# Kernel optimization log

Hardware: AMD Instinct MI355X
Metric: run time of the kernel (lower is better)

## Reference

```python
import jax, jax.numpy as jnp
import numpy as np

DIM = 3072
KV_DIM = 2048
HEADS = 16
DIM_HEAD = 128
INNER = HEADS * DIM_HEAD  # 2048
EPS = 1e-5


def layer_norm(x, g, b):
    mu = jnp.mean(x, axis=-1, keepdims=True)
    var = jnp.var(x, axis=-1, keepdims=True)
    return (x - mu) * jax.lax.rsqrt(var + EPS) * g + b


def setup_inputs() -> dict:
    key = jax.random.key(0)
    ks = jax.random.split(key, 8)
    b, n1, n2 = 2, 2048, 2048
    x = jax.random.normal(ks[0], (b, n1, KV_DIM), dtype=jnp.float32)
    latents = jax.random.normal(ks[1], (b, n2, DIM), dtype=jnp.float32)
    w_q = jax.random.normal(ks[2], (DIM, INNER), dtype=jnp.float32) / np.sqrt(DIM)
    w_kv = jax.random.normal(ks[3], (KV_DIM, 2 * INNER), dtype=jnp.float32) / np.sqrt(KV_DIM)
    w_out = jax.random.normal(ks[4], (INNER, DIM), dtype=jnp.float32) / np.sqrt(INNER)
    ln1_g = jnp.ones((KV_DIM,), jnp.float32)
    ln1_b = jnp.zeros((KV_DIM,), jnp.float32)
    ln2_g = jnp.ones((DIM,), jnp.float32)
    ln2_b = jnp.zeros((DIM,), jnp.float32)
    return {"x": x, "latents": latents, "w_q": w_q, "w_kv": w_kv,
            "w_out": w_out, "ln1_g": ln1_g, "ln1_b": ln1_b,
            "ln2_g": ln2_g, "ln2_b": ln2_b}


def reference(x, latents, w_q, w_kv, w_out, ln1_g, ln1_b, ln2_g, ln2_b):
    b, n2, _ = latents.shape
    xn = layer_norm(x, ln1_g, ln1_b)            # (b, n1, kv_dim)
    ln = layer_norm(latents, ln2_g, ln2_b)      # (b, n2, dim)
    q = ln @ w_q                                # (b, n2, inner)
    kv = xn @ w_kv                              # (b, n1, 2*inner)
    k, v = jnp.split(kv, 2, axis=-1)
    # (b, h, n, d)
    def split_heads(t):
        bs, n, _ = t.shape
        return t.reshape(bs, n, HEADS, DIM_HEAD).transpose(0, 2, 1, 3)
    q, k, v = split_heads(q), split_heads(k), split_heads(v)
    scale = 1.0 / np.sqrt(np.sqrt(DIM_HEAD)).astype(np.float32)
    w = jnp.einsum('bhqd,bhkd->bhqk', q * scale, k * scale)
    w = jax.nn.softmax(w.astype(jnp.float32), axis=-1).astype(q.dtype)
    out = jnp.einsum('bhqk,bhkd->bhqd', w, v)
    out = out.transpose(0, 2, 1, 3).reshape(b, n2, INNER)
    return out @ w_out
```

## Files before the change

kernel.cpp:

```cpp
#include <hip/hip_runtime.h>
#include <type_traits>


using u16 = unsigned short;
using u32 = unsigned int;
typedef __attribute__((ext_vector_type(8))) short short8;
typedef __attribute__((ext_vector_type(4))) float floatx4;

typedef __attribute__((address_space(1))) const unsigned int gu32;
typedef __attribute__((address_space(3))) unsigned int lu32;

__device__ __forceinline__ void gld16(void* lds, const void* g) {
  __builtin_amdgcn_global_load_lds((gu32*)g, (lu32*)lds, 16, 0, 0);
}

__device__ inline u16 f2bf(float f) {
  u32 u = __float_as_uint(f);
  u32 r = (u + 0x7FFFu + ((u >> 16) & 1u)) >> 16;
  return (u16)r;
}

template <int L>
__global__ __launch_bounds__(256) void ln_cast(const float* __restrict__ in,
                                               const float* __restrict__ gw,
                                               const float* __restrict__ bw,
                                               u16* __restrict__ out) {
  constexpr int C4 = L / 1024;
  const int row = blockIdx.x;
  const int t = threadIdx.x;
  const float* rp = in + (size_t)row * L;
  float4 v[C4];
  float s = 0.f, ss = 0.f;
#pragma unroll
  for (int c = 0; c < C4; ++c) {
    v[c] = *(const float4*)(rp + (c * 256 + t) * 4);
    s += v[c].x + v[c].y + v[c].z + v[c].w;
    ss += v[c].x * v[c].x + v[c].y * v[c].y + v[c].z * v[c].z + v[c].w * v[c].w;
  }
#pragma unroll
  for (int off = 32; off > 0; off >>= 1) {
    s += __shfl_down(s, off);
    ss += __shfl_down(ss, off);
  }
  __shared__ float red[8];
  const int wave = t >> 6, lane = t & 63;
  if (lane == 0) { red[wave] = s; red[4 + wave] = ss; }
  __syncthreads();
  const float tot = red[0] + red[1] + red[2] + red[3];
  const float tss = red[4] + red[5] + red[6] + red[7];
  const float mu = tot * (1.f / L);
  const float rstd = rsqrtf(tss * (1.f / L) - mu * mu + 1e-5f);
  u16* op = out + (size_t)row * L;
#pragma unroll
  for (int c = 0; c < C4; ++c) {
    const int base = (c * 256 + t) * 4;
    float4 gv = *(const float4*)(gw + base);
    float4 bv = *(const float4*)(bw + base);
    u32 p0 = (u32)f2bf((v[c].x - mu) * rstd * gv.x + bv.x) |
             ((u32)f2bf((v[c].y - mu) * rstd * gv.y + bv.y) << 16);
    u32 p1 = (u32)f2bf((v[c].z - mu) * rstd * gv.z + bv.z) |
             ((u32)f2bf((v[c].w - mu) * rstd * gv.w + bv.w) << 16);
    uint2 pk; pk.x = p0; pk.y = p1;
    *(uint2*)(op + base) = pk;
  }
}

__global__ __launch_bounds__(256) void transpose_cast(const float* __restrict__ in,
                                                      u16* __restrict__ out,
                                                      int R, int C) {
  __shared__ u16 tile[32][33];
  const int c0 = blockIdx.x * 32, r0 = blockIdx.y * 32;
  const int x = threadIdx.x, y = threadIdx.y;
#pragma unroll
  for (int j = 0; j < 4; ++j)
    tile[y + 8 * j][x] = f2bf(in[(size_t)(r0 + y + 8 * j) * C + c0 + x]);
  __syncthreads();
#pragma unroll
  for (int j = 0; j < 4; ++j)
    out[(size_t)(c0 + y + 8 * j) * R + r0 + x] = tile[x][y + 8 * j];
}

__global__ __launch_bounds__(256) void transpose_v(const u16* __restrict__ kvb,
                                                   u16* __restrict__ vT) {
  __shared__ u16 tile[32][33];
  const int bh = blockIdx.z, b = bh >> 4, h = bh & 15;
  const u16* src = kvb + (size_t)b * 2048 * 4096 + 2048 + h * 128;
  u16* dst = vT + (size_t)bh * 128 * 2048;
  const int d0 = blockIdx.x * 32, n0 = blockIdx.y * 32;
  const int x = threadIdx.x, y = threadIdx.y;
#pragma unroll
  for (int j = 0; j < 4; ++j)
    tile[y + 8 * j][x] = src[(size_t)(n0 + y + 8 * j) * 4096 + d0 + x];
  __syncthreads();
#pragma unroll
  for (int j = 0; j < 4; ++j)
    dst[(size_t)(d0 + y + 8 * j) * 2048 + n0 + x] = tile[x][y + 8 * j];
}

template <typename OutT>
__global__ __launch_bounds__(256) void gemm_bt(const u16* __restrict__ A,
                                               const u16* __restrict__ Bt,
                                               OutT* __restrict__ C,
                                               int M, int N, int K) {
  __shared__ u16 As[128 * 64];
  __shared__ u16 Bs[128 * 64];
  const int tid = threadIdx.x;
  const int wave = tid >> 6, lane = tid & 63, l16 = lane & 15, quad = lane >> 4;
  const int wm = (wave >> 1) * 64, wn = (wave & 1) * 64;
  const long m0 = (long)blockIdx.y * 128, n0 = (long)blockIdx.x * 128;
  const int srow = tid >> 3;
  const int gc = ((tid & 7) ^ ((tid >> 3) & 7)) * 8;
  const u16* Ag0 = A + (m0 + srow) * (long)K + gc;
  const u16* Bg0 = Bt + (n0 + srow) * (long)K + gc;
  const long rowoff = 32L * K;

  const floatx4 fz = {0.f, 0.f, 0.f, 0.f};
  floatx4 acc[4][4];
#pragma unroll
  for (int i = 0; i < 4; ++i)
#pragma unroll
    for (int j = 0; j < 4; ++j) acc[i][j] = fz;

  for (int k0 = 0; k0 < K; k0 += 64) {
    __syncthreads();
#pragma unroll
    for (int c = 0; c < 4; ++c) {
      gld16(&As[(c * 256 + tid) * 8], Ag0 + c * rowoff + k0);
      gld16(&Bs[(c * 256 + tid) * 8], Bg0 + c * rowoff + k0);
    }
    __syncthreads();
#pragma unroll
    for (int kd = 0; kd < 2; ++kd) {
      const int sw = ((4 * kd + quad) ^ (l16 & 7)) * 8;
      short8 a[4], b[4];
#pragma unroll
      for (int i = 0; i < 4; ++i) a[i] = *(const short8*)&As[(wm + i * 16 + l16) * 64 + sw];
#pragma unroll
      for (int j = 0; j < 4; ++j) b[j] = *(const short8*)&Bs[(wn + j * 16 + l16) * 64 + sw];
#pragma unroll
      for (int i = 0; i < 4; ++i)
#pragma unroll
        for (int j = 0; j < 4; ++j)
          acc[i][j] = __builtin_amdgcn_mfma_f32_16x16x32_bf16(a[i], b[j], acc[i][j], 0, 0, 0);
    }
  }

#pragma unroll
  for (int i = 0; i < 4; ++i)
#pragma unroll
    for (int r = 0; r < 4; ++r) {
      const long row = m0 + wm + i * 16 + quad * 4 + r;
#pragma unroll
      for (int j = 0; j < 4; ++j) {
        const long col = n0 + wn + j * 16 + l16;
        if constexpr (std::is_same<OutT, float>::value)
          C[row * N + col] = acc[i][j][r];
        else
          C[row * N + col] = f2bf(acc[i][j][r]);
      }
    }
}

__global__ __launch_bounds__(256, 2) void flash_attn(const u16* __restrict__ Q,
                                                     const u16* __restrict__ KV,
                                                     const u16* __restrict__ VT,
                                                     u16* __restrict__ O) {
  __shared__ u16 Ks[2][64 * 128];
  __shared__ u16 Vs[2][128 * 64];
  __shared__ u16 Ps[4][32 * 64];
  const int tid = threadIdx.x;
  const int wave = tid >> 6, lane = tid & 63, l16 = lane & 15, quad = lane >> 4;
  const int d = blockIdx.x;
  const int bh = (d & 7) * 4 + ((d >> 3) & 3);
  const int qt = d >> 5;
  const int b = bh >> 4, h = bh & 15;
  const u16* Qb = Q + (size_t)b * 2048 * 2048 + h * 128;
  const u16* Kb = KV + (size_t)b * 2048 * 4096 + h * 128;
  const u16* Vb = VT + (size_t)bh * 128 * 2048;
  u16* Ob = O + (size_t)b * 2048 * 2048 + h * 128;
  const int q0 = qt * 128 + wave * 32;

  short8 qf[2][4];
#pragma unroll
  for (int t = 0; t < 2; ++t)
#pragma unroll
    for (int kd = 0; kd < 4; ++kd)
      qf[t][kd] = *(const short8*)&Qb[(size_t)(q0 + t * 16 + l16) * 2048 + kd * 32 + quad * 8];

  short8 onesf;
  {
    union { short8 s; u32 w[4]; } uo;
    const u32 o = (l16 == 0) ? 0x3F803F80u : 0u;
#pragma unroll
    for (int i = 0; i < 4; ++i) uo.w[i] = o;
    onesf = uo.s;
  }

  const floatx4 fz = {0.f, 0.f, 0.f, 0.f};
  floatx4 oacc[2][9];
  float m[2][4];
#pragma unroll
  for (int t = 0; t < 2; ++t) {
#pragma unroll
    for (int jd = 0; jd < 9; ++jd) oacc[t][jd] = fz;
#pragma unroll
    for (int r = 0; r < 4; ++r) m[t][r] = -1e30f;
  }

  u16* Psw = Ps[wave];
  const float sc2 = 0.12751775f;

  auto stage = [&](int buf, int kv0) {
#pragma unroll
    for (int c = 0; c < 4; ++c) {
      const int li = c * 256 + tid;
      const int krow = li >> 4, kdb = (li & 15) ^ (krow & 15);
      gld16(&Ks[buf][li * 8], Kb + (size_t)(kv0 + krow) * 4096 + kdb * 8);
      const int vrow = li >> 3, vdb = (li & 7) ^ (vrow & 7);
      gld16(&Vs[buf][li * 8], Vb + (size_t)vrow * 2048 + kv0 + vdb * 8);
    }
  };

  stage(0, 0);
  int cur = 0;

  for (int kt = 0; kt < 32; ++kt) {
    __syncthreads();
    if (kt < 31) stage(cur ^ 1, (kt + 1) * 64);
    const u16* Kc = Ks[cur];
    const u16* Vc = Vs[cur];

    floatx4 sacc[2][4];
#pragma unroll
    for (int t = 0; t < 2; ++t)
#pragma unroll
      for (int jn = 0; jn < 4; ++jn) sacc[t][jn] = fz;
#pragma unroll
    for (int jn = 0; jn < 4; ++jn)
#pragma unroll
      for (int kd = 0; kd < 4; ++kd) {
        short8 kb = *(const short8*)&Kc[(jn * 16 + l16) * 128 + ((4 * kd + quad) ^ l16) * 8];
        sacc[0][jn] = __builtin_amdgcn_mfma_f32_16x16x32_bf16(qf[0][kd], kb, sacc[0][jn], 0, 0, 0);
        sacc[1][jn] = __builtin_amdgcn_mfma_f32_16x16x32_bf16(qf[1][kd], kb, sacc[1][jn], 0, 0, 0);
      }

#pragma unroll
    for (int t = 0; t < 2; ++t) {
#pragma unroll
      for (int r = 0; r < 4; ++r) {
        float mx = fmaxf(fmaxf(sacc[t][0][r], sacc[t][1][r]),
                         fmaxf(sacc[t][2][r], sacc[t][3][r]));
#pragma unroll
        for (int off = 8; off > 0; off >>= 1) mx = fmaxf(mx, __shfl_xor(mx, off, 16));
        const float mnew = fmaxf(m[t][r], sc2 * mx);
        const float alpha = __builtin_amdgcn_exp2f(m[t][r] - mnew);
        m[t][r] = mnew;
        const int q = t * 16 + quad * 4 + r;
        const int mask = (q & 7) ^ (q >> 3);
        u16* prow = &Psw[q * 64 + (l16 & 7)];
#pragma unroll
        for (int jn = 0; jn < 4; ++jn) {
          const float p = __builtin_amdgcn_exp2f(fmaf(sc2, sacc[t][jn][r], -mnew));
          const int slot = (2 * jn + (l16 >> 3)) ^ mask;
          prow[slot * 8] = f2bf(p);
        }
#pragma unroll
        for (int jd = 0; jd < 9; ++jd) oacc[t][jd][r] *= alpha;
      }
    }

    const int pmask0 = (l16 & 7) ^ (l16 >> 3);
    const int pmask1 = (l16 & 7) ^ (2 + (l16 >> 3));
#pragma unroll
    for (int kk = 0; kk < 2; ++kk) {
      const int chunk = 4 * kk + quad;
      short8 pf0 = *(const short8*)&Psw[(l16) * 64 + (chunk ^ pmask0) * 8];
      short8 pf1 = *(const short8*)&Psw[(16 + l16) * 64 + (chunk ^ pmask1) * 8];
#pragma unroll
      for (int jd = 0; jd < 8; ++jd) {
        short8 vb = *(const short8*)&Vc[(jd * 16 + l16) * 64 + (chunk ^ (l16 & 7)) * 8];
        oacc[0][jd] = __builtin_amdgcn_mfma_f32_16x16x32_bf16(pf0, vb, oacc[0][jd], 0, 0, 0);
        oacc[1][jd] = __builtin_amdgcn_mfma_f32_16x16x32_bf16(pf1, vb, oacc[1][jd], 0, 0, 0);
      }
      oacc[0][8] = __builtin_amdgcn_mfma_f32_16x16x32_bf16(pf0, onesf, oacc[0][8], 0, 0, 0);
      oacc[1][8] = __builtin_amdgcn_mfma_f32_16x16x32_bf16(pf1, onesf, oacc[1][8], 0, 0, 0);
    }
    cur ^= 1;
  }

#pragma unroll
  for (int t = 0; t < 2; ++t)
#pragma unroll
    for (int r = 0; r < 4; ++r) {
      const float l = __shfl(oacc[t][8][r], lane & 48);
      const float inv = 1.f / l;
      const size_t row = q0 + t * 16 + quad * 4 + r;
#pragma unroll
      for (int jd = 0; jd < 8; ++jd)
        Ob[row * 2048 + jd * 16 + l16] = f2bf(oacc[t][jd][r] * inv);
    }
}

extern "C" void kernel_launch(void* const* d_in, const int* in_sizes, int n_in,
                              void* d_out, int out_size, void* d_ws, size_t ws_size,
                              hipStream_t stream) {
  const float* x       = (const float*)d_in[0];
  const float* latents = (const float*)d_in[1];
  const float* w_q     = (const float*)d_in[2];
  const float* w_kv    = (const float*)d_in[3];
  const float* w_out   = (const float*)d_in[4];
  const float* ln1_g   = (const float*)d_in[5];
  const float* ln1_b   = (const float*)d_in[6];
  const float* ln2_g   = (const float*)d_in[7];
  const float* ln2_b   = (const float*)d_in[8];

  char* ws = (char*)d_ws;
  u16* xn    = (u16*)(ws);
  u16* lnl   = (u16*)(ws + 16777216);
  u16* wqT   = (u16*)(ws + 41943040);
  u16* wkvT  = (u16*)(ws + 54525952);
  u16* woutT = (u16*)(ws + 71303168);
  u16* qb    = (u16*)(ws + 83886080);
  u16* kvb   = (u16*)(ws + 100663296);
  u16* vTb   = lnl;
  u16* attn  = xn;

  ln_cast<2048><<<dim3(4096), 256, 0, stream>>>(x, ln1_g, ln1_b, xn);
  ln_cast<3072><<<dim3(4096), 256, 0, stream>>>(latents, ln2_g, ln2_b, lnl);

  transpose_cast<<<dim3(64, 96), dim3(32, 8), 0, stream>>>(w_q, wqT, 3072, 2048);
  transpose_cast<<<dim3(128, 64), dim3(32, 8), 0, stream>>>(w_kv, wkvT, 2048, 4096);
  transpose_cast<<<dim3(96, 64), dim3(32, 8), 0, stream>>>(w_out, woutT, 2048, 3072);

  gemm_bt<u16><<<dim3(16, 32), 256, 0, stream>>>(lnl, wqT, qb, 4096, 2048, 3072);
  gemm_bt<u16><<<dim3(32, 32), 256, 0, stream>>>(xn, wkvT, kvb, 4096, 4096, 2048);

  transpose_v<<<dim3(4, 64, 32), dim3(32, 8), 0, stream>>>(kvb, vTb);

  flash_attn<<<dim3(512), 256, 0, stream>>>(qb, kvb, vTb, attn);

  gemm_bt<float><<<dim3(24, 32), 256, 0, stream>>>(attn, woutT, (float*)d_out, 4096, 3072, 2048);
}
```

Baseline: 571.8 us.

## Shrink flash attention tiles to 16 query rows per wave and 32-key blocks

Restructures the attention kernel so each wave handles 16 query rows instead of 32, and each KV block covers 32 keys instead of 64. LDS swizzles are adjusted to match. Block count doubles, and launch bounds now ask for 4 blocks per CU to raise occupancy and fill 256 CUs. The trade-off is that each K/V tile is reused across half as many query rows, which doubles K/V traffic, and there are twice as many loop iterations and syncs.

New measurement: 617.6 us. +8.0%, slower.

```diff
diff --git a/kernel.cpp b/kernel.cpp
--- a/kernel.cpp
+++ b/kernel.cpp
@@ -161,13 +161,13 @@
     }
 }
 
-__global__ __launch_bounds__(256, 2) void flash_attn(const u16* __restrict__ Q,
+__global__ __launch_bounds__(256, 4) void flash_attn(const u16* __restrict__ Q,
                                                      const u16* __restrict__ KV,
                                                      const u16* __restrict__ VT,
                                                      u16* __restrict__ O) {
-  __shared__ u16 Ks[2][64 * 128];
-  __shared__ u16 Vs[2][128 * 64];
-  __shared__ u16 Ps[4][32 * 64];
+  __shared__ u16 Ks[2][32 * 128];
+  __shared__ u16 Vs[2][128 * 32];
+  __shared__ u16 Ps[4][16 * 32];
   const int tid = threadIdx.x;
   const int wave = tid >> 6, lane = tid & 63, l16 = lane & 15, quad = lane >> 4;
   const int d = blockIdx.x;
@@ -178,14 +178,12 @@
   const u16* Kb = KV + (size_t)b * 2048 * 4096 + h * 128;
   const u16* Vb = VT + (size_t)bh * 128 * 2048;
   u16* Ob = O + (size_t)b * 2048 * 2048 + h * 128;
-  const int q0 = qt * 128 + wave * 32;
-
-  short8 qf[2][4];
-#pragma unroll
-  for (int t = 0; t < 2; ++t)
-#pragma unroll
-    for (int kd = 0; kd < 4; ++kd)
-      qf[t][kd] = *(const short8*)&Qb[(size_t)(q0 + t * 16 + l16) * 2048 + kd * 32 + quad * 8];
+  const int q0 = qt * 64 + wave * 16;
+
+  short8 qf[4];
+#pragma unroll
+  for (int kd = 0; kd < 4; ++kd)
+    qf[kd] = *(const short8*)&Qb[(size_t)(q0 + l16) * 2048 + kd * 32 + quad * 8];
 
   short8 onesf;
   {
@@ -197,26 +195,24 @@
   }
 
   const floatx4 fz = {0.f, 0.f, 0.f, 0.f};
-  floatx4 oacc[2][9];
-  float m[2][4];
-#pragma unroll
-  for (int t = 0; t < 2; ++t) {
-#pragma unroll
-    for (int jd = 0; jd < 9; ++jd) oacc[t][jd] = fz;
-#pragma unroll
-    for (int r = 0; r < 4; ++r) m[t][r] = -1e30f;
-  }
+  floatx4 oacc[9];
+  float m[4];
+#pragma unroll
+  for (int jd = 0; jd < 9; ++jd) oacc[jd] = fz;
+#pragma unroll
+  for (int r = 0; r < 4; ++r) m[r] = -1e30f;
 
   u16* Psw = Ps[wave];
   const float sc2 = 0.12751775f;
+  const int sread = (l16 >> 1) & 3;
 
   auto stage = [&](int buf, int kv0) {
 #pragma unroll
-    for (int c = 0; c < 4; ++c) {
+    for (int c = 0; c < 2; ++c) {
       const int li = c * 256 + tid;
       const int krow = li >> 4, kdb = (li & 15) ^ (krow & 15);
       gld16(&Ks[buf][li * 8], Kb + (size_t)(kv0 + krow) * 4096 + kdb * 8);
-      const int vrow = li >> 3, vdb = (li & 7) ^ (vrow & 7);
+      const int vrow = li >> 2, vdb = (li & 3) ^ ((vrow >> 1) & 3);
       gld16(&Vs[buf][li * 8], Vb + (size_t)vrow * 2048 + kv0 + vdb * 8);
     }
   };
@@ -224,81 +220,63 @@
   stage(0, 0);
   int cur = 0;
 
-  for (int kt = 0; kt < 32; ++kt) {
+  for (int kt = 0; kt < 64; ++kt) {
     __syncthreads();
-    if (kt < 31) stage(cur ^ 1, (kt + 1) * 64);
+    if (kt < 63) stage(cur ^ 1, (kt + 1) * 32);
     const u16* Kc = Ks[cur];
     const u16* Vc = Vs[cur];
 
-    floatx4 sacc[2][4];
-#pragma unroll
-    for (int t = 0; t < 2; ++t)
-#pragma unroll
-      for (int jn = 0; jn < 4; ++jn) sacc[t][jn] = fz;
-#pragma unroll
-    for (int jn = 0; jn < 4; ++jn)
+    floatx4 sacc[2];
+#pragma unroll
+    for (int jn = 0; jn < 2; ++jn) sacc[jn] = fz;
+#pragma unroll
+    for (int jn = 0; jn < 2; ++jn)
 #pragma unroll
       for (int kd = 0; kd < 4; ++kd) {
         short8 kb = *(const short8*)&Kc[(jn * 16 + l16) * 128 + ((4 * kd + quad) ^ l16) * 8];
-        sacc[0][jn] = __builtin_amdgcn_mfma_f32_16x16x32_bf16(qf[0][kd], kb, sacc[0][jn], 0, 0, 0);
-        sacc[1][jn] = __builtin_amdgcn_mfma_f32_16x16x32_bf16(qf[1][kd], kb, sacc[1][jn], 0, 0, 0);
+        sacc[jn] = __builtin_amdgcn_mfma_f32_16x16x32_bf16(qf[kd], kb, sacc[jn], 0, 0, 0);
       }
 
 #pragma unroll
-    for (int t = 0; t < 2; ++t) {
-#pragma unroll
-      for (int r = 0; r < 4; ++r) {
-        float mx = fmaxf(fmaxf(sacc[t][0][r], sacc[t][1][r]),
-                         fmaxf(sacc[t][2][r], sacc[t][3][r]));
-#pragma unroll
-        for (int off = 8; off > 0; off >>= 1) mx = fmaxf(mx, __shfl_xor(mx, off, 16));
-        const float mnew = fmaxf(m[t][r], sc2 * mx);
-        const float alpha = __builtin_amdgcn_exp2f(m[t][r] - mnew);
-        m[t][r] = mnew;
-        const int q = t * 16 + quad * 4 + r;
-        const int mask = (q & 7) ^ (q >> 3);
-        u16* prow = &Psw[q * 64 + (l16 & 7)];
-#pragma unroll
-        for (int jn = 0; jn < 4; ++jn) {
-          const float p = __builtin_amdgcn_exp2f(fmaf(sc2, sacc[t][jn][r], -mnew));
-          const int slot = (2 * jn + (l16 >> 3)) ^ mask;
-          prow[slot * 8] = f2bf(p);
-        }
-#pragma unroll
-        for (int jd = 0; jd < 9; ++jd) oacc[t][jd][r] *= alpha;
+    for (int r = 0; r < 4; ++r) {
+      float mx = fmaxf(sacc[0][r], sacc[1][r]);
+#pragma unroll
+      for (int off = 8; off > 0; off >>= 1) mx = fmaxf(mx, __shfl_xor(mx, off, 16));
+      const float mnew = fmaxf(m[r], sc2 * mx);
+      const float alpha = __builtin_amdgcn_exp2f(m[r] - mnew);
+      m[r] = mnew;
+      const int q = quad * 4 + r;
+      const int mask = (q >> 1) & 3;
+      u16* prow = &Psw[q * 32 + (l16 & 7)];
+#pragma unroll
+      for (int jn = 0; jn < 2; ++jn) {
+        const float p = __builtin_amdgcn_exp2f(fmaf(sc2, sacc[jn][r], -mnew));
+        const int slot = (2 * jn + (l16 >> 3)) ^ mask;
+        prow[slot * 8] = f2bf(p);
       }
-    }
-
-    const int pmask0 = (l16 & 7) ^ (l16 >> 3);
-    const int pmask1 = (l16 & 7) ^ (2 + (l16 >> 3));
-#pragma unroll
-    for (int kk = 0; kk < 2; ++kk) {
-      const int chunk = 4 * kk + quad;
-      short8 pf0 = *(const short8*)&Psw[(l16) * 64 + (chunk ^ pmask0) * 8];
-      short8 pf1 = *(const short8*)&Psw[(16 + l16) * 64 + (chunk ^ pmask1) * 8];
-#pragma unroll
-      for (int jd = 0; jd < 8; ++jd) {
-        short8 vb = *(const short8*)&Vc[(jd * 16 + l16) * 64 + (chunk ^ (l16 & 7)) * 8];
-        oacc[0][jd] = __builtin_amdgcn_mfma_f32_16x16x32_bf16(pf0, vb, oacc[0][jd], 0, 0, 0);
-        oacc[1][jd] = __builtin_amdgcn_mfma_f32_16x16x32_bf16(pf1, vb, oacc[1][jd], 0, 0, 0);
-      }
-      oacc[0][8] = __builtin_amdgcn_mfma_f32_16x16x32_bf16(pf0, onesf, oacc[0][8], 0, 0, 0);
-      oacc[1][8] = __builtin_amdgcn_mfma_f32_16x16x32_bf16(pf1, onesf, oacc[1][8], 0, 0, 0);
-    }
+#pragma unroll
+      for (int jd = 0; jd < 9; ++jd) oacc[jd][r] *= alpha;
+    }
+
+    short8 pf = *(const short8*)&Psw[l16 * 32 + (quad ^ ((l16 >> 1) & 3)) * 8];
+#pragma unroll
+    for (int jd = 0; jd < 8; ++jd) {
+      short8 vb = *(const short8*)&Vc[(jd * 16 + l16) * 32 + (quad ^ sread) * 8];
+      oacc[jd] = __builtin_amdgcn_mfma_f32_16x16x32_bf16(pf, vb, oacc[jd], 0, 0, 0);
+    }
+    oacc[8] = __builtin_amdgcn_mfma_f32_16x16x32_bf16(pf, onesf, oacc[8], 0, 0, 0);
     cur ^= 1;
   }
 
 #pragma unroll
-  for (int t = 0; t < 2; ++t)
-#pragma unroll
-    for (int r = 0; r < 4; ++r) {
-      const float l = __shfl(oacc[t][8][r], lane & 48);
-      const float inv = 1.f / l;
-      const size_t row = q0 + t * 16 + quad * 4 + r;
-#pragma unroll
-      for (int jd = 0; jd < 8; ++jd)
-        Ob[row * 2048 + jd * 16 + l16] = f2bf(oacc[t][jd][r] * inv);
-    }
+  for (int r = 0; r < 4; ++r) {
+    const float l = __shfl(oacc[8][r], lane & 48);
+    const float inv = 1.f / l;
+    const size_t row = q0 + quad * 4 + r;
+#pragma unroll
+    for (int jd = 0; jd < 8; ++jd)
+      Ob[row * 2048 + jd * 16 + l16] = f2bf(oacc[jd][r] * inv);
+  }
 }
 
 extern "C" void kernel_launch(void* const* d_in, const int* in_sizes, int n_in,
@@ -337,7 +315,7 @@
 
   transpose_v<<<dim3(4, 64, 32), dim3(32, 8), 0, stream>>>(kvb, vTb);
 
-  flash_attn<<<dim3(512), 256, 0, stream>>>(qb, kvb, vTb, attn);
+  flash_attn<<<dim3(1024), 256, 0, stream>>>(qb, kvb, vTb, attn);
 
   gemm_bt<float><<<dim3(24, 32), 256, 0, stream>>>(attn, woutT, (float*)d_out, 4096, 3072, 2048);
 }
```
